# Kernel tuning notes

Hardware: AMD Instinct MI355X
Metric: run time of the kernel (lower is better)

The kernel has to match this reference:

```python
import jax, jax.numpy as jnp
import numpy as np

B, SQ, SK, D = 32, 2048, 2048, 64

def setup_inputs() -> dict:
    key = jax.random.key(0)
    kq, kk, kv = jax.random.split(key, 3)
    q = jax.random.normal(kq, (B, SQ, D), dtype=jnp.float32)
    k = jax.random.normal(kk, (B, SK, D), dtype=jnp.float32)
    v = jax.random.normal(kv, (B, SK, D), dtype=jnp.float32)
    return {"q": q, "k": k, "v": v}

def reference(q, k, v):
    # Faithful to the torch module: softmax/dropout are defined in __init__
    # but NEVER applied in forward. attn = (q @ k^T) / sqrt(d); out = attn @ v.
    scale = jnp.sqrt(jnp.asarray(k.shape[-1], dtype=jnp.float32))
    attn = jnp.einsum('bqd,bkd->bqk', q, k) / scale  # [B, Sq, Sk]
    out = jnp.einsum('bqk,bkd->bqd', attn, v)        # [B, Sq, Dv]
    return (out, attn)
```

## Files before the change

kernel.cpp:

```cpp
#include <hip/hip_runtime.h>
#include <hip/hip_bf16.h>


typedef __attribute__((ext_vector_type(4))) float        f32x4;
typedef __attribute__((ext_vector_type(8))) short        s16x8;
typedef __attribute__((ext_vector_type(2))) unsigned int u32x2;
typedef __attribute__((ext_vector_type(4))) unsigned int u32x4;

#define NB    32
#define SQL   2048
#define SKL   2048
#define DD    64
#define QBLK  128
#define KBLK  64
#define NTILES (SKL / KBLK)

#define KOFF 0
#define VOFF 16384
#define SOFF 32768

__device__ __forceinline__ unsigned short f2bf(float f) {
    union { float f; unsigned u; } x; x.f = f;
    unsigned r = x.u + 0x7FFFu + ((x.u >> 16) & 1u);
    return (unsigned short)(r >> 16);
}
__device__ __forceinline__ unsigned swzK(unsigned k) { return (k & 7u) << 4; }
__device__ __forceinline__ unsigned swzV(unsigned d) { return (d & 7u) << 4; }
__device__ __forceinline__ unsigned swzS(unsigned q) { return ((q + (q >> 3)) & 7u) << 4; }

__device__ __forceinline__ void bar_lds() {
    asm volatile("s_waitcnt lgkmcnt(0)" ::: "memory");
    __builtin_amdgcn_s_barrier();
    asm volatile("" ::: "memory");
}

__global__ __launch_bounds__(512, 4)
void sdpa_fused(const float* __restrict__ qg, const float* __restrict__ kg,
                const float* __restrict__ vg, float* __restrict__ og,
                float* __restrict__ ag) {
    __shared__ __align__(16) char smem[49152];

    const unsigned tid  = threadIdx.x;
    const unsigned wid  = tid >> 6;
    const unsigned lane = tid & 63u;
    const unsigned l15  = lane & 15u;
    const unsigned l4   = lane >> 4;

    const unsigned xcd = blockIdx.x & 7u;
    const unsigned loc = blockIdx.x >> 3;
    const unsigned b   = xcd * 4u + (loc >> 4);
    const unsigned qt  = loc & 15u;
    const unsigned qbase = qt * QBLK;

    const unsigned kr = tid >> 3, kc = tid & 7u;
    const unsigned vt = tid >> 4, vc = tid & 15u;

    s16x8 aq[2];
    {
        const float* qrow = qg + ((size_t)b * SQL + qbase + wid * 16 + l15) * DD;
        #pragma unroll
        for (int ks = 0; ks < 2; ++ks) {
            f32x4 f0 = *(const f32x4*)(qrow + ks * 32 + l4 * 8);
            f32x4 f1 = *(const f32x4*)(qrow + ks * 32 + l4 * 8 + 4);
            #pragma unroll
            for (int j = 0; j < 4; ++j) {
                aq[ks][j]     = (short)f2bf(f0[j] * 0.125f);
                aq[ks][j + 4] = (short)f2bf(f1[j] * 0.125f);
            }
        }
    }

    f32x4 acc_o[4];
    #pragma unroll
    for (int n = 0; n < 4; ++n) acc_o[n] = (f32x4){0.f, 0.f, 0.f, 0.f};

    const float* kbat = kg + (size_t)b * SKL * DD;
    const float* vbat = vg + (size_t)b * SKL * DD;

    auto stage = [&](int kt, int sel) {
        const float* ksrc = kbat + (size_t)kt * KBLK * DD;
        const float* vsrc = vbat + (size_t)kt * KBLK * DD;
        f32x4 k0 = *(const f32x4*)(ksrc + kr * DD + kc * 8);
        f32x4 k1 = *(const f32x4*)(ksrc + kr * DD + kc * 8 + 4);
        s16x8 h;
        #pragma unroll
        for (int j = 0; j < 4; ++j) {
            h[j]     = (short)f2bf(k0[j]);
            h[j + 4] = (short)f2bf(k1[j]);
        }
        *(s16x8*)(smem + KOFF + sel * 8192 + kr * 128 + ((kc * 16) ^ swzK(kr))) = h;
        f32x4 v0 = *(const f32x4*)(vsrc + (2 * vt) * DD + vc * 4);
        f32x4 v1 = *(const f32x4*)(vsrc + (2 * vt + 1) * DD + vc * 4);
        #pragma unroll
        for (int j = 0; j < 4; ++j) {
            unsigned d = vc * 4 + (unsigned)j;
            unsigned pack = (unsigned)f2bf(v0[j]) | ((unsigned)f2bf(v1[j]) << 16);
            *(unsigned*)(smem + VOFF + sel * 8192 + d * 128 + ((vt * 4) ^ swzV(d))) = pack;
        }
    };

    stage(0, 0);
    bar_lds();

    char* sbase = smem + SOFF + wid * 2048;
    const unsigned rr = lane >> 3, cc = lane & 7u;

    for (int kt = 0; kt < NTILES; ++kt) {
        const int cur = kt & 1;
        if (kt + 1 < NTILES) stage(kt + 1, cur ^ 1);

        const char* kb = smem + KOFF + cur * 8192;
        f32x4 acc[4];
        #pragma unroll
        for (int n = 0; n < 4; ++n) acc[n] = (f32x4){0.f, 0.f, 0.f, 0.f};
        #pragma unroll
        for (int ks = 0; ks < 2; ++ks)
            #pragma unroll
            for (int nk = 0; nk < 4; ++nk) {
                unsigned row = nk * 16 + l15;
                s16x8 bk = *(const s16x8*)(kb + row * 128 +
                            ((ks * 64 + l4 * 16) ^ swzK(row)));
                acc[nk] = __builtin_amdgcn_mfma_f32_16x16x32_bf16(
                              aq[ks], bk, acc[nk], 0, 0, 0);
            }

        #pragma unroll
        for (int nk = 0; nk < 4; ++nk)
            #pragma unroll
            for (int i = 0; i < 4; ++i) {
                unsigned q = l4 * 4 + (unsigned)i;
                unsigned key = nk * 16 + l15;
                *(unsigned short*)(sbase + q * 128 + ((key * 2) ^ swzS(q))) =
                    f2bf(acc[nk][i]);
            }

        {
            float* abase = ag + ((size_t)b * SQL + qbase + wid * 16) * SKL
                              + (size_t)kt * KBLK;
            #pragma unroll
            for (int h = 0; h < 4; ++h) {
                unsigned q  = (h & 1) * 8 + rr;
                unsigned k4 = (h >> 1) * 32 + cc * 4;
                u32x2 p = *(const u32x2*)(sbase + q * 128 + ((k4 * 2) ^ swzS(q)));
                u32x4 w;
                w[0] = p[0] << 16; w[1] = p[0] & 0xFFFF0000u;
                w[2] = p[1] << 16; w[3] = p[1] & 0xFFFF0000u;
                __builtin_nontemporal_store(w,
                    (u32x4*)(abase + (size_t)q * SKL + k4));
            }
        }

        const char* vb = smem + VOFF + cur * 8192;
        #pragma unroll
        for (int ks = 0; ks < 2; ++ks) {
            s16x8 sa = *(const s16x8*)(sbase + l15 * 128 +
                        ((ks * 64 + l4 * 16) ^ swzS(l15)));
            #pragma unroll
            for (int nd = 0; nd < 4; ++nd) {
                unsigned row = nd * 16 + l15;
                s16x8 vf = *(const s16x8*)(vb + row * 128 +
                            ((ks * 64 + l4 * 16) ^ swzV(row)));
                acc_o[nd] = __builtin_amdgcn_mfma_f32_16x16x32_bf16(
                                sa, vf, acc_o[nd], 0, 0, 0);
            }
        }

        bar_lds();
    }

    float* op = og + ((size_t)b * SQL + qbase + wid * 16 + l4 * 4) * DD + l15;
    #pragma unroll
    for (int nd = 0; nd < 4; ++nd)
        #pragma unroll
        for (int i = 0; i < 4; ++i)
            __builtin_nontemporal_store(acc_o[nd][i], op + (size_t)i * DD + nd * 16);
}

extern "C" void kernel_launch(void* const* d_in, const int* in_sizes, int n_in,
                              void* d_out, int out_size, void* d_ws, size_t ws_size,
                              hipStream_t stream) {
    const float* q = (const float*)d_in[0];
    const float* k = (const float*)d_in[1];
    const float* v = (const float*)d_in[2];
    float* outp  = (float*)d_out;
    float* attnp = outp + (size_t)NB * SQL * DD;
    sdpa_fused<<<dim3(NB * (SQL / QBLK)), dim3(512), 0, stream>>>(q, k, v, outp, attnp);
}
```

Baseline: 129.0 us.

## Switch to 32x32 MFMA tiles with key-split waves and direct attn stores

```diff
diff --git a/kernel.cpp b/kernel.cpp
--- a/kernel.cpp
+++ b/kernel.cpp
@@ -2,10 +2,9 @@
 #include <hip/hip_bf16.h>
 
 
-typedef __attribute__((ext_vector_type(4))) float        f32x4;
-typedef __attribute__((ext_vector_type(8))) short        s16x8;
-typedef __attribute__((ext_vector_type(2))) unsigned int u32x2;
-typedef __attribute__((ext_vector_type(4))) unsigned int u32x4;
+typedef __attribute__((ext_vector_type(4)))  float        f32x4;
+typedef __attribute__((ext_vector_type(16))) float        f32x16;
+typedef __attribute__((ext_vector_type(8)))  short        s16x8;
 
 #define NB    32
 #define SQL   2048
@@ -26,7 +25,7 @@
 }
 __device__ __forceinline__ unsigned swzK(unsigned k) { return (k & 7u) << 4; }
 __device__ __forceinline__ unsigned swzV(unsigned d) { return (d & 7u) << 4; }
-__device__ __forceinline__ unsigned swzS(unsigned q) { return ((q + (q >> 3)) & 7u) << 4; }
+__device__ __forceinline__ unsigned swzS(unsigned q) { return ((q >> 2) & 1u) << 5; }
 
 __device__ __forceinline__ void bar_lds() {
     asm volatile("s_waitcnt lgkmcnt(0)" ::: "memory");
@@ -45,6 +44,10 @@
     const unsigned lane = tid & 63u;
     const unsigned l15  = lane & 15u;
     const unsigned l4   = lane >> 4;
+    const unsigned l31  = lane & 31u;
+    const unsigned l5   = lane >> 5;
+    const unsigned qw   = wid >> 1;
+    const unsigned kh   = wid & 1u;
 
     const unsigned xcd = blockIdx.x & 7u;
     const unsigned loc = blockIdx.x >> 3;
@@ -55,24 +58,26 @@
     const unsigned kr = tid >> 3, kc = tid & 7u;
     const unsigned vt = tid >> 4, vc = tid & 15u;
 
-    s16x8 aq[2];
+    s16x8 qf[4];
     {
-        const float* qrow = qg + ((size_t)b * SQL + qbase + wid * 16 + l15) * DD;
+        const float* qrow = qg + (size_t)(b * SQL + qbase + qw * 32 + l31) * DD;
         #pragma unroll
-        for (int ks = 0; ks < 2; ++ks) {
-            f32x4 f0 = *(const f32x4*)(qrow + ks * 32 + l4 * 8);
-            f32x4 f1 = *(const f32x4*)(qrow + ks * 32 + l4 * 8 + 4);
+        for (int kk = 0; kk < 4; ++kk) {
+            f32x4 f0 = *(const f32x4*)(qrow + kk * 16 + l5 * 8);
+            f32x4 f1 = *(const f32x4*)(qrow + kk * 16 + l5 * 8 + 4);
             #pragma unroll
             for (int j = 0; j < 4; ++j) {
-                aq[ks][j]     = (short)f2bf(f0[j] * 0.125f);
-                aq[ks][j + 4] = (short)f2bf(f1[j] * 0.125f);
+                qf[kk][j]     = (short)f2bf(f0[j] * 0.125f);
+                qf[kk][j + 4] = (short)f2bf(f1[j] * 0.125f);
             }
         }
     }
 
-    f32x4 acc_o[4];
+    f32x4 acc_o[2][4];
     #pragma unroll
-    for (int n = 0; n < 4; ++n) acc_o[n] = (f32x4){0.f, 0.f, 0.f, 0.f};
+    for (int m = 0; m < 2; ++m)
+        #pragma unroll
+        for (int n = 0; n < 4; ++n) acc_o[m][n] = (f32x4){0.f, 0.f, 0.f, 0.f};
 
     const float* kbat = kg + (size_t)b * SKL * DD;
     const float* vbat = vg + (size_t)b * SKL * DD;
@@ -102,78 +107,84 @@
     stage(0, 0);
     bar_lds();
 
-    char* sbase = smem + SOFF + wid * 2048;
-    const unsigned rr = lane >> 3, cc = lane & 7u;
+    char* sb = smem + SOFF + wid * 2048;
+    float* const aw = ag + (size_t)(b * SQL + qbase + qw * 32 + 4 * l5) * SKL
+                         + kh * 32 + l31;
 
     for (int kt = 0; kt < NTILES; ++kt) {
         const int cur = kt & 1;
         if (kt + 1 < NTILES) stage(kt + 1, cur ^ 1);
 
         const char* kb = smem + KOFF + cur * 8192;
-        f32x4 acc[4];
+        f32x16 an = {0,0,0,0,0,0,0,0,0,0,0,0,0,0,0,0};
         #pragma unroll
-        for (int n = 0; n < 4; ++n) acc[n] = (f32x4){0.f, 0.f, 0.f, 0.f};
-        #pragma unroll
-        for (int ks = 0; ks < 2; ++ks)
+        for (int kk = 0; kk < 4; ++kk) {
+            unsigned row = kh * 32 + l31;
+            s16x8 kf = *(const s16x8*)(kb + row * 128 +
+                        ((kk * 32 + l5 * 16) ^ swzK(row)));
+            an = __builtin_amdgcn_mfma_f32_32x32x16_bf16(qf[kk], kf, an, 0, 0, 0);
+        }
+
+        {
+            float* ap = aw + (size_t)kt * KBLK;
             #pragma unroll
-            for (int nk = 0; nk < 4; ++nk) {
-                unsigned row = nk * 16 + l15;
-                s16x8 bk = *(const s16x8*)(kb + row * 128 +
-                            ((ks * 64 + l4 * 16) ^ swzK(row)));
-                acc[nk] = __builtin_amdgcn_mfma_f32_16x16x32_bf16(
-                              aq[ks], bk, acc[nk], 0, 0, 0);
-            }
+            for (int r = 0; r < 16; ++r)
+                __builtin_nontemporal_store(an[r],
+                    ap + (size_t)((r & 3) + 8 * (r >> 2)) * SKL);
+        }
 
         #pragma unroll
-        for (int nk = 0; nk < 4; ++nk)
-            #pragma unroll
-            for (int i = 0; i < 4; ++i) {
-                unsigned q = l4 * 4 + (unsigned)i;
-                unsigned key = nk * 16 + l15;
-                *(unsigned short*)(sbase + q * 128 + ((key * 2) ^ swzS(q))) =
-                    f2bf(acc[nk][i]);
-            }
-
-        {
-            float* abase = ag + ((size_t)b * SQL + qbase + wid * 16) * SKL
-                              + (size_t)kt * KBLK;
-            #pragma unroll
-            for (int h = 0; h < 4; ++h) {
-                unsigned q  = (h & 1) * 8 + rr;
-                unsigned k4 = (h >> 1) * 32 + cc * 4;
-                u32x2 p = *(const u32x2*)(sbase + q * 128 + ((k4 * 2) ^ swzS(q)));
-                u32x4 w;
-                w[0] = p[0] << 16; w[1] = p[0] & 0xFFFF0000u;
-                w[2] = p[1] << 16; w[3] = p[1] & 0xFFFF0000u;
-                __builtin_nontemporal_store(w,
-                    (u32x4*)(abase + (size_t)q * SKL + k4));
-            }
+        for (int r = 0; r < 16; ++r) {
+            unsigned q = (r & 3) + 8 * (r >> 2) + 4 * l5;
+            *(unsigned short*)(sb + q * 64 + ((l31 * 2) ^ swzS(q))) = f2bf(an[r]);
         }
 
         const char* vb = smem + VOFF + cur * 8192;
         #pragma unroll
-        for (int ks = 0; ks < 2; ++ks) {
-            s16x8 sa = *(const s16x8*)(sbase + l15 * 128 +
-                        ((ks * 64 + l4 * 16) ^ swzS(l15)));
+        for (int m = 0; m < 2; ++m) {
+            unsigned q = m * 16 + l15;
+            s16x8 sa = *(const s16x8*)(sb + q * 64 + ((l4 * 16) ^ swzS(q)));
             #pragma unroll
             for (int nd = 0; nd < 4; ++nd) {
                 unsigned row = nd * 16 + l15;
                 s16x8 vf = *(const s16x8*)(vb + row * 128 +
-                            ((ks * 64 + l4 * 16) ^ swzV(row)));
-                acc_o[nd] = __builtin_amdgcn_mfma_f32_16x16x32_bf16(
-                                sa, vf, acc_o[nd], 0, 0, 0);
+                            ((kh * 64 + l4 * 16) ^ swzV(row)));
+                acc_o[m][nd] = __builtin_amdgcn_mfma_f32_16x16x32_bf16(
+                                   sa, vf, acc_o[m][nd], 0, 0, 0);
             }
         }
 
         bar_lds();
     }
 
-    float* op = og + ((size_t)b * SQL + qbase + wid * 16 + l4 * 4) * DD + l15;
-    #pragma unroll
-    for (int nd = 0; nd < 4; ++nd)
+    float* red = (float*)smem + qw * 2048;
+    if (kh == 1) {
         #pragma unroll
-        for (int i = 0; i < 4; ++i)
-            __builtin_nontemporal_store(acc_o[nd][i], op + (size_t)i * DD + nd * 16);
+        for (int m = 0; m < 2; ++m)
+            #pragma unroll
+            for (int nd = 0; nd < 4; ++nd)
+                #pragma unroll
+                for (int i = 0; i < 4; ++i) {
+                    unsigned q = m * 16 + l4 * 4 + (unsigned)i;
+                    unsigned d = nd * 16 + l15;
+                    red[q * 64 + d] = acc_o[m][nd][i];
+                }
+    }
+    bar_lds();
+    if (kh == 0) {
+        float* op = og + (size_t)(b * SQL + qbase + qw * 32) * DD;
+        #pragma unroll
+        for (int m = 0; m < 2; ++m)
+            #pragma unroll
+            for (int nd = 0; nd < 4; ++nd)
+                #pragma unroll
+                for (int i = 0; i < 4; ++i) {
+                    unsigned q = m * 16 + l4 * 4 + (unsigned)i;
+                    unsigned d = nd * 16 + l15;
+                    float v = acc_o[m][nd][i] + red[q * 64 + d];
+                    __builtin_nontemporal_store(v, op + (size_t)q * DD + d);
+                }
+    }
 }
 
 extern "C" void kernel_launch(void* const* d_in, const int* in_sizes, int n_in,
```

Result: slower. 138.8 us (+7.6%).

## Halve query tile and split key tile across wave pairs with LDS reduction

Applied to the files above, without the earlier changes.

```diff
diff --git a/kernel.cpp b/kernel.cpp
--- a/kernel.cpp
+++ b/kernel.cpp
@@ -11,7 +11,7 @@
 #define SQL   2048
 #define SKL   2048
 #define DD    64
-#define QBLK  128
+#define QBLK  64
 #define KBLK  64
 #define NTILES (SKL / KBLK)
 
@@ -26,7 +26,7 @@
 }
 __device__ __forceinline__ unsigned swzK(unsigned k) { return (k & 7u) << 4; }
 __device__ __forceinline__ unsigned swzV(unsigned d) { return (d & 7u) << 4; }
-__device__ __forceinline__ unsigned swzS(unsigned q) { return ((q + (q >> 3)) & 7u) << 4; }
+__device__ __forceinline__ unsigned swzS(unsigned q) { return ((q >> 2) & 3u) << 4; }
 
 __device__ __forceinline__ void bar_lds() {
     asm volatile("s_waitcnt lgkmcnt(0)" ::: "memory");
@@ -34,22 +34,24 @@
     asm volatile("" ::: "memory");
 }
 
-__global__ __launch_bounds__(512, 4)
+__global__ __launch_bounds__(512, 8)
 void sdpa_fused(const float* __restrict__ qg, const float* __restrict__ kg,
                 const float* __restrict__ vg, float* __restrict__ og,
                 float* __restrict__ ag) {
-    __shared__ __align__(16) char smem[49152];
+    __shared__ __align__(16) char smem[40960];
 
     const unsigned tid  = threadIdx.x;
     const unsigned wid  = tid >> 6;
     const unsigned lane = tid & 63u;
     const unsigned l15  = lane & 15u;
     const unsigned l4   = lane >> 4;
+    const unsigned qh   = wid >> 1;
+    const unsigned kh   = wid & 1u;
 
     const unsigned xcd = blockIdx.x & 7u;
     const unsigned loc = blockIdx.x >> 3;
-    const unsigned b   = xcd * 4u + (loc >> 4);
-    const unsigned qt  = loc & 15u;
+    const unsigned b   = xcd * 4u + (loc >> 5);
+    const unsigned qt  = loc & 31u;
     const unsigned qbase = qt * QBLK;
 
     const unsigned kr = tid >> 3, kc = tid & 7u;
@@ -57,7 +59,7 @@
 
     s16x8 aq[2];
     {
-        const float* qrow = qg + ((size_t)b * SQL + qbase + wid * 16 + l15) * DD;
+        const float* qrow = qg + ((size_t)b * SQL + qbase + qh * 16 + l15) * DD;
         #pragma unroll
         for (int ks = 0; ks < 2; ++ks) {
             f32x4 f0 = *(const f32x4*)(qrow + ks * 32 + l4 * 8);
@@ -102,46 +104,46 @@
     stage(0, 0);
     bar_lds();
 
-    char* sbase = smem + SOFF + wid * 2048;
+    char* sb = smem + SOFF + wid * 1024;
     const unsigned rr = lane >> 3, cc = lane & 7u;
+    float* const aw = ag + ((size_t)b * SQL + qbase + qh * 16) * SKL + kh * 32;
 
     for (int kt = 0; kt < NTILES; ++kt) {
         const int cur = kt & 1;
         if (kt + 1 < NTILES) stage(kt + 1, cur ^ 1);
 
         const char* kb = smem + KOFF + cur * 8192;
-        f32x4 acc[4];
-        #pragma unroll
-        for (int n = 0; n < 4; ++n) acc[n] = (f32x4){0.f, 0.f, 0.f, 0.f};
+        f32x4 acc[2];
+        acc[0] = (f32x4){0.f, 0.f, 0.f, 0.f};
+        acc[1] = (f32x4){0.f, 0.f, 0.f, 0.f};
         #pragma unroll
         for (int ks = 0; ks < 2; ++ks)
             #pragma unroll
-            for (int nk = 0; nk < 4; ++nk) {
-                unsigned row = nk * 16 + l15;
-                s16x8 bk = *(const s16x8*)(kb + row * 128 +
-                            ((ks * 64 + l4 * 16) ^ swzK(row)));
+            for (int nk = 0; nk < 2; ++nk) {
+                unsigned key = kh * 32 + nk * 16 + l15;
+                s16x8 bk = *(const s16x8*)(kb + key * 128 +
+                            ((ks * 64 + l4 * 16) ^ swzK(key)));
                 acc[nk] = __builtin_amdgcn_mfma_f32_16x16x32_bf16(
                               aq[ks], bk, acc[nk], 0, 0, 0);
             }
 
         #pragma unroll
-        for (int nk = 0; nk < 4; ++nk)
+        for (int nk = 0; nk < 2; ++nk)
             #pragma unroll
             for (int i = 0; i < 4; ++i) {
-                unsigned q = l4 * 4 + (unsigned)i;
+                unsigned q   = l4 * 4 + (unsigned)i;
                 unsigned key = nk * 16 + l15;
-                *(unsigned short*)(sbase + q * 128 + ((key * 2) ^ swzS(q))) =
+                *(unsigned short*)(sb + q * 64 + ((key * 2) ^ swzS(q))) =
                     f2bf(acc[nk][i]);
             }
 
         {
-            float* abase = ag + ((size_t)b * SQL + qbase + wid * 16) * SKL
-                              + (size_t)kt * KBLK;
-            #pragma unroll
-            for (int h = 0; h < 4; ++h) {
-                unsigned q  = (h & 1) * 8 + rr;
-                unsigned k4 = (h >> 1) * 32 + cc * 4;
-                u32x2 p = *(const u32x2*)(sbase + q * 128 + ((k4 * 2) ^ swzS(q)));
+            float* abase = aw + (size_t)kt * KBLK;
+            #pragma unroll
+            for (int h = 0; h < 2; ++h) {
+                unsigned q  = h * 8 + rr;
+                unsigned k4 = cc * 4;
+                u32x2 p = *(const u32x2*)(sb + q * 64 + ((k4 * 2) ^ swzS(q)));
                 u32x4 w;
                 w[0] = p[0] << 16; w[1] = p[0] & 0xFFFF0000u;
                 w[2] = p[1] << 16; w[3] = p[1] & 0xFFFF0000u;
@@ -151,29 +153,43 @@
         }
 
         const char* vb = smem + VOFF + cur * 8192;
-        #pragma unroll
-        for (int ks = 0; ks < 2; ++ks) {
-            s16x8 sa = *(const s16x8*)(sbase + l15 * 128 +
-                        ((ks * 64 + l4 * 16) ^ swzS(l15)));
-            #pragma unroll
-            for (int nd = 0; nd < 4; ++nd) {
-                unsigned row = nd * 16 + l15;
-                s16x8 vf = *(const s16x8*)(vb + row * 128 +
-                            ((ks * 64 + l4 * 16) ^ swzV(row)));
-                acc_o[nd] = __builtin_amdgcn_mfma_f32_16x16x32_bf16(
-                                sa, vf, acc_o[nd], 0, 0, 0);
-            }
+        s16x8 sa = *(const s16x8*)(sb + l15 * 64 + ((l4 * 16) ^ swzS(l15)));
+        #pragma unroll
+        for (int nd = 0; nd < 4; ++nd) {
+            unsigned vrow = nd * 16 + l15;
+            s16x8 vf = *(const s16x8*)(vb + vrow * 128 +
+                        ((kh * 64 + l4 * 16) ^ swzV(vrow)));
+            acc_o[nd] = __builtin_amdgcn_mfma_f32_16x16x32_bf16(
+                            sa, vf, acc_o[nd], 0, 0, 0);
         }
 
         bar_lds();
     }
 
-    float* op = og + ((size_t)b * SQL + qbase + wid * 16 + l4 * 4) * DD + l15;
-    #pragma unroll
-    for (int nd = 0; nd < 4; ++nd)
-        #pragma unroll
-        for (int i = 0; i < 4; ++i)
-            __builtin_nontemporal_store(acc_o[nd][i], op + (size_t)i * DD + nd * 16);
+    float* red = (float*)smem + qh * 1024;
+    if (kh == 1) {
+        #pragma unroll
+        for (int nd = 0; nd < 4; ++nd)
+            #pragma unroll
+            for (int i = 0; i < 4; ++i) {
+                unsigned q = l4 * 4 + (unsigned)i;
+                unsigned d = nd * 16 + l15;
+                red[q * 64 + d] = acc_o[nd][i];
+            }
+    }
+    bar_lds();
+    if (kh == 0) {
+        float* op = og + ((size_t)b * SQL + qbase + qh * 16) * DD;
+        #pragma unroll
+        for (int nd = 0; nd < 4; ++nd)
+            #pragma unroll
+            for (int i = 0; i < 4; ++i) {
+                unsigned q = l4 * 4 + (unsigned)i;
+                unsigned d = nd * 16 + l15;
+                float v = acc_o[nd][i] + red[q * 64 + d];
+                __builtin_nontemporal_store(v, op + (size_t)q * DD + d);
+            }
+    }
 }
 
 extern "C" void kernel_launch(void* const* d_in, const int* in_sizes, int n_in,
```

After: 130.1 us. No clear change (+0.9%).

## Batch attn-matrix stores across four key tiles into full-row 1KB writes

Applied to the files above, without the earlier changes.

```diff
diff --git a/kernel.cpp b/kernel.cpp
--- a/kernel.cpp
+++ b/kernel.cpp
@@ -103,69 +103,81 @@
     bar_lds();
 
     char* sbase = smem + SOFF + wid * 2048;
-    const unsigned rr = lane >> 3, cc = lane & 7u;
-
-    for (int kt = 0; kt < NTILES; ++kt) {
-        const int cur = kt & 1;
-        if (kt + 1 < NTILES) stage(kt + 1, cur ^ 1);
-
-        const char* kb = smem + KOFF + cur * 8192;
-        f32x4 acc[4];
-        #pragma unroll
-        for (int n = 0; n < 4; ++n) acc[n] = (f32x4){0.f, 0.f, 0.f, 0.f};
-        #pragma unroll
-        for (int ks = 0; ks < 2; ++ks)
-            #pragma unroll
-            for (int nk = 0; nk < 4; ++nk) {
-                unsigned row = nk * 16 + l15;
-                s16x8 bk = *(const s16x8*)(kb + row * 128 +
-                            ((ks * 64 + l4 * 16) ^ swzK(row)));
-                acc[nk] = __builtin_amdgcn_mfma_f32_16x16x32_bf16(
-                              aq[ks], bk, acc[nk], 0, 0, 0);
-            }
-
-        #pragma unroll
-        for (int nk = 0; nk < 4; ++nk)
-            #pragma unroll
-            for (int i = 0; i < 4; ++i) {
-                unsigned q = l4 * 4 + (unsigned)i;
-                unsigned key = nk * 16 + l15;
-                *(unsigned short*)(sbase + q * 128 + ((key * 2) ^ swzS(q))) =
-                    f2bf(acc[nk][i]);
-            }
-
-        {
-            float* abase = ag + ((size_t)b * SQL + qbase + wid * 16) * SKL
-                              + (size_t)kt * KBLK;
-            #pragma unroll
-            for (int h = 0; h < 4; ++h) {
-                unsigned q  = (h & 1) * 8 + rr;
-                unsigned k4 = (h >> 1) * 32 + cc * 4;
-                u32x2 p = *(const u32x2*)(sbase + q * 128 + ((k4 * 2) ^ swzS(q)));
-                u32x4 w;
-                w[0] = p[0] << 16; w[1] = p[0] & 0xFFFF0000u;
-                w[2] = p[1] << 16; w[3] = p[1] & 0xFFFF0000u;
-                __builtin_nontemporal_store(w,
-                    (u32x4*)(abase + (size_t)q * SKL + k4));
-            }
-        }
-
-        const char* vb = smem + VOFF + cur * 8192;
-        #pragma unroll
-        for (int ks = 0; ks < 2; ++ks) {
-            s16x8 sa = *(const s16x8*)(sbase + l15 * 128 +
-                        ((ks * 64 + l4 * 16) ^ swzS(l15)));
-            #pragma unroll
-            for (int nd = 0; nd < 4; ++nd) {
-                unsigned row = nd * 16 + l15;
-                s16x8 vf = *(const s16x8*)(vb + row * 128 +
-                            ((ks * 64 + l4 * 16) ^ swzV(row)));
-                acc_o[nd] = __builtin_amdgcn_mfma_f32_16x16x32_bf16(
-                                sa, vf, acc_o[nd], 0, 0, 0);
-            }
-        }
-
-        bar_lds();
+    const unsigned grp = lane >> 4;
+    const unsigned xk  = lane & 15u;
+    float* const awave = ag + ((size_t)b * SQL + qbase + wid * 16) * SKL;
+
+    u32x2 pbuf[16];
+
+    for (int ktg = 0; ktg < NTILES / 4; ++ktg) {
+        #pragma unroll
+        for (int j = 0; j < 4; ++j) {
+            const int kt  = ktg * 4 + j;
+            const int cur = j & 1;
+            if (kt + 1 < NTILES) stage(kt + 1, cur ^ 1);
+
+            const char* kb = smem + KOFF + cur * 8192;
+            f32x4 acc[4];
+            #pragma unroll
+            for (int n = 0; n < 4; ++n) acc[n] = (f32x4){0.f, 0.f, 0.f, 0.f};
+            #pragma unroll
+            for (int ks = 0; ks < 2; ++ks)
+                #pragma unroll
+                for (int nk = 0; nk < 4; ++nk) {
+                    unsigned row = nk * 16 + l15;
+                    s16x8 bk = *(const s16x8*)(kb + row * 128 +
+                                ((ks * 64 + l4 * 16) ^ swzK(row)));
+                    acc[nk] = __builtin_amdgcn_mfma_f32_16x16x32_bf16(
+                                  aq[ks], bk, acc[nk], 0, 0, 0);
+                }
+
+            #pragma unroll
+            for (int nk = 0; nk < 4; ++nk)
+                #pragma unroll
+                for (int i = 0; i < 4; ++i) {
+                    unsigned q = l4 * 4 + (unsigned)i;
+                    unsigned key = nk * 16 + l15;
+                    *(unsigned short*)(sbase + q * 128 + ((key * 2) ^ swzS(q))) =
+                        f2bf(acc[nk][i]);
+                }
+
+            if (grp == (unsigned)j) {
+                #pragma unroll
+                for (int r = 0; r < 16; ++r)
+                    pbuf[r] = *(const u32x2*)(sbase + r * 128 +
+                               ((xk * 8) ^ swzS((unsigned)r)));
+            }
+
+            if (j == 3) {
+                float* abase = awave + (size_t)ktg * 256;
+                #pragma unroll
+                for (int r = 0; r < 16; ++r) {
+                    u32x2 p = pbuf[r];
+                    u32x4 w;
+                    w[0] = p[0] << 16; w[1] = p[0] & 0xFFFF0000u;
+                    w[2] = p[1] << 16; w[3] = p[1] & 0xFFFF0000u;
+                    __builtin_nontemporal_store(w,
+                        (u32x4*)(abase + (size_t)r * SKL + lane * 4));
+                }
+            }
+
+            const char* vb = smem + VOFF + cur * 8192;
+            #pragma unroll
+            for (int ks = 0; ks < 2; ++ks) {
+                s16x8 sa = *(const s16x8*)(sbase + l15 * 128 +
+                            ((ks * 64 + l4 * 16) ^ swzS(l15)));
+                #pragma unroll
+                for (int nd = 0; nd < 4; ++nd) {
+                    unsigned row = nd * 16 + l15;
+                    s16x8 vf = *(const s16x8*)(vb + row * 128 +
+                                ((ks * 64 + l4 * 16) ^ swzV(row)));
+                    acc_o[nd] = __builtin_amdgcn_mfma_f32_16x16x32_bf16(
+                                    sa, vf, acc_o[nd], 0, 0, 0);
+                }
+            }
+
+            bar_lds();
+        }
     }
 
     float* op = og + ((size_t)b * SQL + qbase + wid * 16 + l4 * 4) * DD + l15;
```

Measured after the change: 145.7 us. 12.9% more time.
